# Optimization experiments

Measured on AMD Instinct MI355X. Metric: run time of the kernel, lower is better.

The kernel has to match this reference:

```python
import jax, jax.numpy as jnp
import numpy as np

N_SEND = 12288   # 12 * 32^2
N_REC = 49152    # 12 * 64^2
E = 196608       # 4 * N_REC (knn with k=4)
D = 256
EIN, EOUT = 4, 256
LIN_IN, LIN_OUT = 512, 256
B = 2


def setup_inputs() -> dict:
    key = jax.random.key(0)
    ks = jax.random.split(key, 12)
    s = 0.05
    x = jax.random.normal(ks[0], (B, N_SEND, D), jnp.float32)
    edge_attr = jax.random.normal(ks[1], (E, EIN), jnp.float32)
    idx_send = jax.random.randint(ks[2], (E,), 0, N_SEND, dtype=jnp.int32)
    idx_rec = jnp.sort(jax.random.randint(ks[3], (E,), 0, N_REC, dtype=jnp.int32))
    return {
        "x": x,
        "edge_attr": edge_attr,
        "idx_send": idx_send,
        "idx_rec": idx_rec,
        "We1": jax.random.normal(ks[4], (EIN, EOUT), jnp.float32) * s,
        "be1": jnp.zeros((EOUT,), jnp.float32),
        "We2": jax.random.normal(ks[5], (EOUT, EOUT), jnp.float32) * s,
        "be2": jnp.zeros((EOUT,), jnp.float32),
        "Wl1": jax.random.normal(ks[6], (LIN_IN, LIN_OUT), jnp.float32) * s,
        "bl1": jnp.zeros((LIN_OUT,), jnp.float32),
        "Wl2": jax.random.normal(ks[7], (LIN_OUT, LIN_OUT), jnp.float32) * s,
        "bl2": jnp.zeros((LIN_OUT,), jnp.float32),
    }


def reference(x, edge_attr, idx_send, idx_rec, We1, be1, We2, be2, Wl1, bl1, Wl2, bl2):
    # edge embedder MLP: Linear -> GELU -> Linear   [E, EOUT]
    ef = jax.nn.gelu(edge_attr @ We1 + be1) @ We2 + be2
    # gather sender node features by edge           [B, E, D]
    v_s = x[:, idx_send, :]
    # concat gathered features with (batch-broadcast) edge embeddings [B, E, D+EOUT]
    ef_b = jnp.broadcast_to(ef[None], (v_s.shape[0],) + ef.shape)
    v_s_prime = jnp.concatenate([v_s, ef_b], axis=-1)
    # scatter_sum over receiver index along edge dim -> [B, N_REC, LIN_IN]
    agg = jax.vmap(lambda m: jax.ops.segment_sum(m, idx_rec, num_segments=N_REC))(v_s_prime)
    # final FeedForward: Linear -> GELU -> Linear
    return jax.nn.gelu(agg @ Wl1 + bl1) @ Wl2 + bl2
```

## Files before the change

kernel.cpp:

```cpp
#include <hip/hip_runtime.h>
#include <hip/hip_bf16.h>

#define N_SEND 12288
#define N_REC  49152
#define NEDGE  196608
#define RECV   48

typedef __attribute__((ext_vector_type(8)))  short short8;
typedef __attribute__((ext_vector_type(4)))  short shortx4;
typedef __attribute__((ext_vector_type(4)))  float floatx4;
typedef __attribute__((ext_vector_type(16))) float floatx16;
typedef __attribute__((ext_vector_type(4)))  unsigned int uintx4;

__device__ inline short f2bs(float f) {
    __hip_bfloat16 h = __float2bfloat16(f);
    return *reinterpret_cast<short*>(&h);
}
__device__ inline float gelu_tanh(float x) {
    const float k0 = 0.7978845608028654f;
    float u = k0 * (x + 0.044715f * x * x * x);
    float e = __expf(2.0f * u);
    float t = 1.0f - 2.0f / (e + 1.0f);
    return 0.5f * x * (1.0f + t);
}

__global__ void prep_kernel(const float* __restrict__ We2, const float* __restrict__ be2,
                            const float* __restrict__ Wl1, const float* __restrict__ Wl2,
                            short* __restrict__ BT1, short* __restrict__ WT2,
                            float* __restrict__ cvec) {
    int i = blockIdx.x;
    int n = threadIdx.x;
    if (i < 256) {
        float acc = 0.f;
        for (int j = 0; j < 256; ++j)
            acc += We2[i * 256 + j] * Wl1[(256 + j) * 256 + n];
        BT1[n * 512 + i]       = f2bs(Wl1[i * 256 + n]);
        BT1[n * 512 + 256 + i] = f2bs(acc);
        WT2[n * 256 + i]       = f2bs(Wl2[i * 256 + n]);
    } else {
        float acc = 0.f;
        for (int j = 0; j < 256; ++j)
            acc += be2[j] * Wl1[(256 + j) * 256 + n];
        cvec[n] = acc;
    }
}

__global__ void xcast_kernel(const float* __restrict__ X, short* __restrict__ Xb) {
    int i = (blockIdx.x * 256 + threadIdx.x) * 8;
    floatx4 v0 = *(const floatx4*)(X + i);
    floatx4 v1 = *(const floatx4*)(X + i + 4);
    short8 p;
#pragma unroll
    for (int j = 0; j < 4; ++j) { p[j] = f2bs(v0[j]); p[j + 4] = f2bs(v1[j]); }
    *(short8*)(Xb + i) = p;
}

__global__ void bounds_kernel(const int* __restrict__ idx_rec, int* __restrict__ bnd) {
    int r = blockIdx.x * 256 + threadIdx.x;
    if (r > N_REC) return;
    int lo = 0, hi = NEDGE;
    while (lo < hi) { int mid = (lo + hi) >> 1; if (idx_rec[mid] < r) lo = mid + 1; else hi = mid; }
    bnd[r] = lo;
}

#define XTU(f, row) ((((f) * 96) + ((row) ^ ((f) & 7))) * 8)
#define HTU(f, rl)  ((((f) * 48) + ((rl) ^ ((f) & 7))) * 8)

__global__ __launch_bounds__(512, 4)
void fused48(const int* __restrict__ idx_send, const int* __restrict__ bnd,
             const float* __restrict__ EA, const float* __restrict__ We1,
             const float* __restrict__ be1, const short* __restrict__ Xb,
             const short* __restrict__ BT1, const short* __restrict__ WT2,
             const float* __restrict__ cvec, const float* __restrict__ bl1,
             const float* __restrict__ bl2, float* __restrict__ OUT) {
    __shared__ __attribute__((aligned(16))) short XT[32 * 96 * 8];
    __shared__ __attribute__((aligned(16))) short HT[32 * 48 * 8];
    __shared__ int sb[RECV + 1];

    int t = threadIdx.x;
    int r0 = blockIdx.x * RECV;
    if (t <= RECV) sb[t] = bnd[r0 + t];
    __syncthreads();

    {
        int cg = t & 31;
        int b  = (t >> 5) & 1;
        int rh = t >> 6;
        int c8 = cg * 8;
        int hc = c8 + 4 * b;

        floatx4 w0 = *(const floatx4*)(We1 + hc);
        floatx4 w1 = *(const floatx4*)(We1 + 256 + hc);
        floatx4 w2 = *(const floatx4*)(We1 + 512 + hc);
        floatx4 w3 = *(const floatx4*)(We1 + 768 + hc);
        floatx4 bb = *(const floatx4*)(be1 + hc);
        const short* xb_t = Xb + (size_t)b * N_SEND * 256 + c8;

#pragma unroll
        for (int r = 0; r < 6; ++r) {
            int rl = rh * 6 + r;
            int es = __builtin_amdgcn_readfirstlane(sb[rl]);
            int ee = __builtin_amdgcn_readfirstlane(sb[rl + 1]);

            float xacc[8];
            float hacc[4];
#pragma unroll
            for (int c = 0; c < 8; ++c) xacc[c] = 0.f;
#pragma unroll
            for (int c = 0; c < 4; ++c) hacc[c] = 0.f;

            int s = 0; floatx4 a = {0.f, 0.f, 0.f, 0.f};
            if (es < ee) { s = idx_send[es]; a = *(const floatx4*)(EA + (size_t)es * 4); }
            for (int e = es; e < ee; ++e) {
                int cs = s; floatx4 ca = a;
                int ep = (e + 1 < ee) ? e + 1 : e;
                s = idx_send[ep];
                a = *(const floatx4*)(EA + (size_t)ep * 4);
                uintx4 xv = *(const uintx4*)(xb_t + (size_t)cs * 256);
#pragma unroll
                for (int dw = 0; dw < 4; ++dw) {
                    xacc[2 * dw]     += __builtin_bit_cast(float, xv[dw] << 16);
                    xacc[2 * dw + 1] += __builtin_bit_cast(float, xv[dw] & 0xffff0000u);
                }
#pragma unroll
                for (int j = 0; j < 4; ++j) {
                    float u = ca[0] * w0[j] + ca[1] * w1[j] + ca[2] * w2[j] + ca[3] * w3[j] + bb[j];
                    hacc[j] += gelu_tanh(u);
                }
            }
            short8 xp;
#pragma unroll
            for (int c = 0; c < 8; ++c) xp[c] = f2bs(xacc[c]);
            *(short8*)(XT + XTU(cg, b * RECV + rl)) = xp;
            shortx4 hp;
#pragma unroll
            for (int c = 0; c < 4; ++c) hp[c] = f2bs(hacc[c]);
            *(shortx4*)(HT + HTU(cg, rl) + 4 * b) = hp;
        }
    }
    __syncthreads();

    int w = t >> 6, lane = t & 63;
    int m = lane & 31, q = lane >> 5;
    int wcol = w * 32;
    floatx16 acc[3];
#pragma unroll
    for (int i = 0; i < 3; ++i)
#pragma unroll
        for (int j = 0; j < 16; ++j) acc[i][j] = 0.f;

    const short* Bp1 = BT1 + (size_t)(wcol + m) * 512 + q * 8;
#pragma unroll
    for (int ci = 0; ci < 8; ++ci) {
#pragma unroll
        for (int kk = 0; kk < 4; ++kk) {
            short8 bv = *(const short8*)(Bp1 + ci * 64 + kk * 16);
            int f = ci * 8 + 2 * kk + q;
            short8 a0, a1, a2;
            if (ci < 4) {
                a0 = *(const short8*)(XT + XTU(f, m));
                a1 = *(const short8*)(XT + XTU(f, 32 + m));
                a2 = *(const short8*)(XT + XTU(f, 64 + m));
            } else {
                int fh = f - 32;
                a0 = *(const short8*)(HT + HTU(fh, m));
                int rl1 = (m < 16) ? 32 + m : m - 16;
                a1 = *(const short8*)(HT + HTU(fh, rl1));
                a2 = *(const short8*)(HT + HTU(fh, 16 + m));
            }
            acc[0] = __builtin_amdgcn_mfma_f32_32x32x16_bf16(bv, a0, acc[0], 0, 0, 0);
            acc[1] = __builtin_amdgcn_mfma_f32_32x32x16_bf16(bv, a1, acc[1], 0, 0, 0);
            acc[2] = __builtin_amdgcn_mfma_f32_32x32x16_bf16(bv, a2, acc[2], 0, 0, 0);
        }
    }
    __syncthreads();

#pragma unroll
    for (int qd = 0; qd < 4; ++qd) {
        int c0 = wcol + qd * 8 + q * 4;
        floatx4 cv  = *(const floatx4*)(cvec + c0);
        floatx4 b1v = *(const floatx4*)(bl1 + c0);
#pragma unroll
        for (int rt = 0; rt < 3; ++rt) {
            int r = rt * 32 + m;
            int bat = (r >= RECV) ? 1 : 0;
            int rl = r - RECV * bat;
            float cntv = (float)(sb[rl + 1] - sb[rl]);
            shortx4 pk;
#pragma unroll
            for (int j = 0; j < 4; ++j)
                pk[j] = f2bs(gelu_tanh(acc[rt][qd * 4 + j] + cntv * cv[j] + b1v[j]));
            *(shortx4*)(XT + XTU(w * 4 + qd, r) + q * 4) = pk;
        }
    }
#pragma unroll
    for (int i = 0; i < 3; ++i)
#pragma unroll
        for (int j = 0; j < 16; ++j) acc[i][j] = 0.f;
    __syncthreads();

    const short* Bp2 = WT2 + (size_t)(wcol + m) * 256 + q * 8;
#pragma unroll
    for (int ci = 0; ci < 4; ++ci) {
#pragma unroll
        for (int kk = 0; kk < 4; ++kk) {
            short8 bv = *(const short8*)(Bp2 + ci * 64 + kk * 16);
            int f2 = ci * 8 + 2 * kk + q;
            short8 a0 = *(const short8*)(XT + XTU(f2, m));
            short8 a1 = *(const short8*)(XT + XTU(f2, 32 + m));
            short8 a2 = *(const short8*)(XT + XTU(f2, 64 + m));
            acc[0] = __builtin_amdgcn_mfma_f32_32x32x16_bf16(bv, a0, acc[0], 0, 0, 0);
            acc[1] = __builtin_amdgcn_mfma_f32_32x32x16_bf16(bv, a1, acc[1], 0, 0, 0);
            acc[2] = __builtin_amdgcn_mfma_f32_32x32x16_bf16(bv, a2, acc[2], 0, 0, 0);
        }
    }

#pragma unroll
    for (int rt = 0; rt < 3; ++rt) {
        int r = rt * 32 + m;
        int bat = (r >= RECV) ? 1 : 0;
        int rl = r - RECV * bat;
        size_t obase = ((size_t)bat * N_REC + r0 + rl) * 256;
#pragma unroll
        for (int qd = 0; qd < 4; ++qd) {
            int c0 = wcol + qd * 8 + q * 4;
            floatx4 bv = *(const floatx4*)(bl2 + c0);
            floatx4 o;
#pragma unroll
            for (int j = 0; j < 4; ++j)
                o[j] = acc[rt][qd * 4 + j] + bv[j];
            *(floatx4*)(OUT + obase + c0) = o;
        }
    }
}

extern "C" void kernel_launch(void* const* d_in, const int* in_sizes, int n_in,
                              void* d_out, int out_size, void* d_ws, size_t ws_size,
                              hipStream_t stream) {
    const float* x        = (const float*)d_in[0];
    const float* ea       = (const float*)d_in[1];
    const int*   idx_send = (const int*)d_in[2];
    const int*   idx_rec  = (const int*)d_in[3];
    const float* We1      = (const float*)d_in[4];
    const float* be1      = (const float*)d_in[5];
    const float* We2      = (const float*)d_in[6];
    const float* be2      = (const float*)d_in[7];
    const float* Wl1      = (const float*)d_in[8];
    const float* bl1      = (const float*)d_in[9];
    const float* Wl2      = (const float*)d_in[10];
    const float* bl2      = (const float*)d_in[11];
    float* out = (float*)d_out;
    char*  ws  = (char*)d_ws;

    short* BT1  = (short*)(ws + 0);
    short* WT2  = (short*)(ws + 262144);
    float* cvec = (float*)(ws + 393216);
    int*   bnd  = (int*)  (ws + 397312);
    short* Xb   = (short*)(ws + 1048576);

    prep_kernel<<<257, 256, 0, stream>>>(We2, be2, Wl1, Wl2, BT1, WT2, cvec);
    xcast_kernel<<<(2 * N_SEND * 256) / (256 * 8), 256, 0, stream>>>(x, Xb);
    bounds_kernel<<<(N_REC + 1 + 255) / 256, 256, 0, stream>>>(idx_rec, bnd);
    fused48<<<N_REC / RECV, 512, 0, stream>>>(idx_send, bnd, ea, We1, be1, Xb,
                                              BT1, WT2, cvec, bl1, bl2, out);
}
```

Before: 280.5 us.

## Flatten per-receiver edge loops into double-buffered 4-edge batches with interleaved X layout

Replaces the per-receiver edge loop, which prefetched one edge ahead, with a single flattened loop over all edges of a thread's six receivers. Edges are loaded in double-buffered batches of four, and partial sums are flushed to shared memory at receiver boundaries. The bf16 copy of x is also re-laid out so both batches of a sender node sit next to each other in one 512-element row, which improves gather locality. The aim is more memory-level parallelism for the irregular gathers, at the cost of more registers, boundary branching, and possible occupancy loss.

```diff
diff --git a/kernel.cpp b/kernel.cpp
--- a/kernel.cpp
+++ b/kernel.cpp
@@ -47,12 +47,16 @@
 
 __global__ void xcast_kernel(const float* __restrict__ X, short* __restrict__ Xb) {
     int i = (blockIdx.x * 256 + threadIdx.x) * 8;
+    int row = i >> 8;
+    int c   = i & 255;
+    int bb_ = (row >= N_SEND) ? 1 : 0;
+    int n   = row - bb_ * N_SEND;
     floatx4 v0 = *(const floatx4*)(X + i);
     floatx4 v1 = *(const floatx4*)(X + i + 4);
     short8 p;
 #pragma unroll
     for (int j = 0; j < 4; ++j) { p[j] = f2bs(v0[j]); p[j + 4] = f2bs(v1[j]); }
-    *(short8*)(Xb + i) = p;
+    *(short8*)(Xb + (size_t)n * 512 + bb_ * 256 + c) = p;
 }
 
 __global__ void bounds_kernel(const int* __restrict__ idx_rec, int* __restrict__ bnd) {
@@ -75,7 +79,7 @@
              const float* __restrict__ bl2, float* __restrict__ OUT) {
     __shared__ __attribute__((aligned(16))) short XT[32 * 96 * 8];
     __shared__ __attribute__((aligned(16))) short HT[32 * 48 * 8];
-    __shared__ int sb[RECV + 1];
+    __shared__ int sb[RECV + 9];
 
     int t = threadIdx.x;
     int r0 = blockIdx.x * RECV;
@@ -94,49 +98,91 @@
         floatx4 w2 = *(const floatx4*)(We1 + 512 + hc);
         floatx4 w3 = *(const floatx4*)(We1 + 768 + hc);
         floatx4 bb = *(const floatx4*)(be1 + hc);
-        const short* xb_t = Xb + (size_t)b * N_SEND * 256 + c8;
-
-#pragma unroll
-        for (int r = 0; r < 6; ++r) {
-            int rl = rh * 6 + r;
-            int es = __builtin_amdgcn_readfirstlane(sb[rl]);
-            int ee = __builtin_amdgcn_readfirstlane(sb[rl + 1]);
-
-            float xacc[8];
-            float hacc[4];
-#pragma unroll
-            for (int c = 0; c < 8; ++c) xacc[c] = 0.f;
-#pragma unroll
-            for (int c = 0; c < 4; ++c) hacc[c] = 0.f;
-
-            int s = 0; floatx4 a = {0.f, 0.f, 0.f, 0.f};
-            if (es < ee) { s = idx_send[es]; a = *(const floatx4*)(EA + (size_t)es * 4); }
-            for (int e = es; e < ee; ++e) {
-                int cs = s; floatx4 ca = a;
-                int ep = (e + 1 < ee) ? e + 1 : e;
-                s = idx_send[ep];
-                a = *(const floatx4*)(EA + (size_t)ep * 4);
-                uintx4 xv = *(const uintx4*)(xb_t + (size_t)cs * 256);
-#pragma unroll
-                for (int dw = 0; dw < 4; ++dw) {
-                    xacc[2 * dw]     += __builtin_bit_cast(float, xv[dw] << 16);
-                    xacc[2 * dw + 1] += __builtin_bit_cast(float, xv[dw] & 0xffff0000u);
-                }
-#pragma unroll
-                for (int j = 0; j < 4; ++j) {
-                    float u = ca[0] * w0[j] + ca[1] * w1[j] + ca[2] * w2[j] + ca[3] * w3[j] + bb[j];
-                    hacc[j] += gelu_tanh(u);
-                }
+        const short* xb_t = Xb + b * 256 + c8;
+
+        int rl0 = rh * 6;
+        int e0 = __builtin_amdgcn_readfirstlane(sb[rl0]);
+        int eN = __builtin_amdgcn_readfirstlane(sb[rl0 + 6]);
+
+        float xacc[8];
+        float hacc[4];
+#pragma unroll
+        for (int c = 0; c < 8; ++c) xacc[c] = 0.f;
+#pragma unroll
+        for (int c = 0; c < 4; ++c) hacc[c] = 0.f;
+
+        int rcur = rl0;
+        int bend = __builtin_amdgcn_readfirstlane(sb[rcur + 1]);
+
+#define FLUSH_R() {                                                          \
+        short8 xp_; shortx4 hp_;                                             \
+        _Pragma("unroll")                                                    \
+        for (int c_ = 0; c_ < 8; ++c_) xp_[c_] = f2bs(xacc[c_]);             \
+        *(short8*)(XT + XTU(cg, b * RECV + rcur)) = xp_;                     \
+        _Pragma("unroll")                                                    \
+        for (int c_ = 0; c_ < 4; ++c_) hp_[c_] = f2bs(hacc[c_]);             \
+        *(shortx4*)(HT + HTU(cg, rcur) + 4 * b) = hp_;                       \
+        _Pragma("unroll")                                                    \
+        for (int c_ = 0; c_ < 8; ++c_) xacc[c_] = 0.f;                       \
+        _Pragma("unroll")                                                    \
+        for (int c_ = 0; c_ < 4; ++c_) hacc[c_] = 0.f;                       \
+        ++rcur;                                                              \
+        bend = __builtin_amdgcn_readfirstlane(sb[rcur + 1]);                 \
+    }
+
+#define LOADC(S, A, XV, base) {                                              \
+        _Pragma("unroll")                                                    \
+        for (int j_ = 0; j_ < 4; ++j_) {                                     \
+            int ei_ = (base) + j_; ei_ = (ei_ < eN) ? ei_ : (eN - 1);        \
+            S[j_] = idx_send[ei_];                                           \
+            A[j_] = *(const floatx4*)(EA + (size_t)ei_ * 4);                 \
+        }                                                                    \
+        _Pragma("unroll")                                                    \
+        for (int j_ = 0; j_ < 4; ++j_)                                       \
+            XV[j_] = *(const uintx4*)(xb_t + (size_t)S[j_] * 512);           \
+    }
+
+#define CONSUME1(av, xvv, ej) {                                              \
+        if ((ej) < eN) {                                                     \
+            while ((ej) == bend) FLUSH_R();                                  \
+            uintx4 xv_ = (xvv);                                              \
+            _Pragma("unroll")                                                \
+            for (int dw_ = 0; dw_ < 4; ++dw_) {                              \
+                xacc[2 * dw_]     += __builtin_bit_cast(float, xv_[dw_] << 16);          \
+                xacc[2 * dw_ + 1] += __builtin_bit_cast(float, xv_[dw_] & 0xffff0000u);  \
+            }                                                                \
+            floatx4 a_ = (av);                                               \
+            _Pragma("unroll")                                                \
+            for (int jj_ = 0; jj_ < 4; ++jj_) {                              \
+                float u_ = a_[0] * w0[jj_] + a_[1] * w1[jj_] + a_[2] * w2[jj_] \
+                         + a_[3] * w3[jj_] + bb[jj_];                        \
+                hacc[jj_] += gelu_tanh(u_);                                  \
+            }                                                                \
+        }                                                                    \
+    }
+
+        if (e0 < eN) {
+            int sA[4], sB[4];
+            floatx4 aA[4], aB[4];
+            uintx4 xvA[4], xvB[4];
+            int e = e0;
+            LOADC(sA, aA, xvA, e);
+            for (;;) {
+                int moreB = (e + 4 < eN);
+                if (moreB) LOADC(sB, aB, xvB, e + 4);
+#pragma unroll
+                for (int j = 0; j < 4; ++j) CONSUME1(aA[j], xvA[j], e + j);
+                e += 4;
+                if (!moreB) break;
+                int moreA = (e + 4 < eN);
+                if (moreA) LOADC(sA, aA, xvA, e + 4);
+#pragma unroll
+                for (int j = 0; j < 4; ++j) CONSUME1(aB[j], xvB[j], e + j);
+                e += 4;
+                if (!moreA) break;
             }
-            short8 xp;
-#pragma unroll
-            for (int c = 0; c < 8; ++c) xp[c] = f2bs(xacc[c]);
-            *(short8*)(XT + XTU(cg, b * RECV + rl)) = xp;
-            shortx4 hp;
-#pragma unroll
-            for (int c = 0; c < 4; ++c) hp[c] = f2bs(hacc[c]);
-            *(shortx4*)(HT + HTU(cg, rl) + 4 * b) = hp;
-        }
+        }
+        while (rcur < rl0 + 6) FLUSH_R();
     }
     __syncthreads();
 
```

New measurement: 274.6 us. 2.1% less time.

## Shrink receiver tile to 16 and interleave batch rows in bf16 node buffer

Applied to the files above, without the earlier changes.

The fused kernel now handles 16 receivers per block instead of 48, so each wave keeps a single 32x32 MFMA tile (16 receivers times 2 batches) and uses a third of the LDS and accumulator registers. The occupancy hint rises to 8 blocks per CU and the grid grows threefold. The bf16 cast of x is also rearranged so both batch rows of a sender node sit next to each other, which places the two gathers for an edge in one 1KB span. In exchange, the GEMM weight matrices are reloaded from global or L2 three times as often per output row, and there are more block launches and barrier overheads.

```diff
diff --git a/kernel.cpp b/kernel.cpp
--- a/kernel.cpp
+++ b/kernel.cpp
@@ -4,7 +4,7 @@
 #define N_SEND 12288
 #define N_REC  49152
 #define NEDGE  196608
-#define RECV   48
+#define RECV   16
 
 typedef __attribute__((ext_vector_type(8)))  short short8;
 typedef __attribute__((ext_vector_type(4)))  short shortx4;
@@ -47,12 +47,16 @@
 
 __global__ void xcast_kernel(const float* __restrict__ X, short* __restrict__ Xb) {
     int i = (blockIdx.x * 256 + threadIdx.x) * 8;
+    int row = i >> 8;
+    int c   = i & 255;
+    int bb_ = (row >= N_SEND) ? 1 : 0;
+    int n   = row - bb_ * N_SEND;
     floatx4 v0 = *(const floatx4*)(X + i);
     floatx4 v1 = *(const floatx4*)(X + i + 4);
     short8 p;
 #pragma unroll
     for (int j = 0; j < 4; ++j) { p[j] = f2bs(v0[j]); p[j + 4] = f2bs(v1[j]); }
-    *(short8*)(Xb + i) = p;
+    *(short8*)(Xb + (size_t)n * 512 + bb_ * 256 + c) = p;
 }
 
 __global__ void bounds_kernel(const int* __restrict__ idx_rec, int* __restrict__ bnd) {
@@ -63,18 +67,18 @@
     bnd[r] = lo;
 }
 
-#define XTU(f, row) ((((f) * 96) + ((row) ^ ((f) & 7))) * 8)
-#define HTU(f, rl)  ((((f) * 48) + ((rl) ^ ((f) & 7))) * 8)
-
-__global__ __launch_bounds__(512, 4)
-void fused48(const int* __restrict__ idx_send, const int* __restrict__ bnd,
+#define XTU(f, row) ((((f) * 32) + ((row) ^ ((f) & 7))) * 8)
+#define HTU(f, rl)  ((((f) * 16) + ((rl) ^ ((f) & 7))) * 8)
+
+__global__ __launch_bounds__(512, 8)
+void fused16(const int* __restrict__ idx_send, const int* __restrict__ bnd,
              const float* __restrict__ EA, const float* __restrict__ We1,
              const float* __restrict__ be1, const short* __restrict__ Xb,
              const short* __restrict__ BT1, const short* __restrict__ WT2,
              const float* __restrict__ cvec, const float* __restrict__ bl1,
              const float* __restrict__ bl2, float* __restrict__ OUT) {
-    __shared__ __attribute__((aligned(16))) short XT[32 * 96 * 8];
-    __shared__ __attribute__((aligned(16))) short HT[32 * 48 * 8];
+    __shared__ __attribute__((aligned(16))) short XT[32 * 32 * 8];
+    __shared__ __attribute__((aligned(16))) short HT[32 * 16 * 8];
     __shared__ int sb[RECV + 1];
 
     int t = threadIdx.x;
@@ -94,11 +98,11 @@
         floatx4 w2 = *(const floatx4*)(We1 + 512 + hc);
         floatx4 w3 = *(const floatx4*)(We1 + 768 + hc);
         floatx4 bb = *(const floatx4*)(be1 + hc);
-        const short* xb_t = Xb + (size_t)b * N_SEND * 256 + c8;
-
-#pragma unroll
-        for (int r = 0; r < 6; ++r) {
-            int rl = rh * 6 + r;
+        const short* xb_t = Xb + b * 256 + c8;
+
+#pragma unroll
+        for (int r = 0; r < 2; ++r) {
+            int rl = rh * 2 + r;
             int es = __builtin_amdgcn_readfirstlane(sb[rl]);
             int ee = __builtin_amdgcn_readfirstlane(sb[rl + 1]);
 
@@ -116,7 +120,7 @@
                 int ep = (e + 1 < ee) ? e + 1 : e;
                 s = idx_send[ep];
                 a = *(const floatx4*)(EA + (size_t)ep * 4);
-                uintx4 xv = *(const uintx4*)(xb_t + (size_t)cs * 256);
+                uintx4 xv = *(const uintx4*)(xb_t + (size_t)cs * 512);
 #pragma unroll
                 for (int dw = 0; dw < 4; ++dw) {
                     xacc[2 * dw]     += __builtin_bit_cast(float, xv[dw] << 16);
@@ -143,11 +147,9 @@
     int w = t >> 6, lane = t & 63;
     int m = lane & 31, q = lane >> 5;
     int wcol = w * 32;
-    floatx16 acc[3];
-#pragma unroll
-    for (int i = 0; i < 3; ++i)
-#pragma unroll
-        for (int j = 0; j < 16; ++j) acc[i][j] = 0.f;
+    floatx16 acc;
+#pragma unroll
+    for (int j = 0; j < 16; ++j) acc[j] = 0.f;
 
     const short* Bp1 = BT1 + (size_t)(wcol + m) * 512 + q * 8;
 #pragma unroll
@@ -156,47 +158,34 @@
         for (int kk = 0; kk < 4; ++kk) {
             short8 bv = *(const short8*)(Bp1 + ci * 64 + kk * 16);
             int f = ci * 8 + 2 * kk + q;
-            short8 a0, a1, a2;
+            short8 a0;
             if (ci < 4) {
                 a0 = *(const short8*)(XT + XTU(f, m));
-                a1 = *(const short8*)(XT + XTU(f, 32 + m));
-                a2 = *(const short8*)(XT + XTU(f, 64 + m));
             } else {
-                int fh = f - 32;
-                a0 = *(const short8*)(HT + HTU(fh, m));
-                int rl1 = (m < 16) ? 32 + m : m - 16;
-                a1 = *(const short8*)(HT + HTU(fh, rl1));
-                a2 = *(const short8*)(HT + HTU(fh, 16 + m));
+                a0 = *(const short8*)(HT + HTU(f - 32, m & 15));
             }
-            acc[0] = __builtin_amdgcn_mfma_f32_32x32x16_bf16(bv, a0, acc[0], 0, 0, 0);
-            acc[1] = __builtin_amdgcn_mfma_f32_32x32x16_bf16(bv, a1, acc[1], 0, 0, 0);
-            acc[2] = __builtin_amdgcn_mfma_f32_32x32x16_bf16(bv, a2, acc[2], 0, 0, 0);
-        }
-    }
-    __syncthreads();
-
-#pragma unroll
-    for (int qd = 0; qd < 4; ++qd) {
-        int c0 = wcol + qd * 8 + q * 4;
-        floatx4 cv  = *(const floatx4*)(cvec + c0);
-        floatx4 b1v = *(const floatx4*)(bl1 + c0);
-#pragma unroll
-        for (int rt = 0; rt < 3; ++rt) {
-            int r = rt * 32 + m;
-            int bat = (r >= RECV) ? 1 : 0;
-            int rl = r - RECV * bat;
-            float cntv = (float)(sb[rl + 1] - sb[rl]);
+            acc = __builtin_amdgcn_mfma_f32_32x32x16_bf16(bv, a0, acc, 0, 0, 0);
+        }
+    }
+    __syncthreads();
+
+    {
+        int rl = m & 15;
+        float cntv = (float)(sb[rl + 1] - sb[rl]);
+#pragma unroll
+        for (int qd = 0; qd < 4; ++qd) {
+            int c0 = wcol + qd * 8 + q * 4;
+            floatx4 cv  = *(const floatx4*)(cvec + c0);
+            floatx4 b1v = *(const floatx4*)(bl1 + c0);
             shortx4 pk;
 #pragma unroll
             for (int j = 0; j < 4; ++j)
-                pk[j] = f2bs(gelu_tanh(acc[rt][qd * 4 + j] + cntv * cv[j] + b1v[j]));
-            *(shortx4*)(XT + XTU(w * 4 + qd, r) + q * 4) = pk;
-        }
-    }
-#pragma unroll
-    for (int i = 0; i < 3; ++i)
-#pragma unroll
-        for (int j = 0; j < 16; ++j) acc[i][j] = 0.f;
+                pk[j] = f2bs(gelu_tanh(acc[qd * 4 + j] + cntv * cv[j] + b1v[j]));
+            *(shortx4*)(XT + XTU(w * 4 + qd, m) + q * 4) = pk;
+        }
+#pragma unroll
+        for (int j = 0; j < 16; ++j) acc[j] = 0.f;
+    }
     __syncthreads();
 
     const short* Bp2 = WT2 + (size_t)(wcol + m) * 256 + q * 8;
@@ -207,19 +196,13 @@
             short8 bv = *(const short8*)(Bp2 + ci * 64 + kk * 16);
             int f2 = ci * 8 + 2 * kk + q;
             short8 a0 = *(const short8*)(XT + XTU(f2, m));
-            short8 a1 = *(const short8*)(XT + XTU(f2, 32 + m));
-            short8 a2 = *(const short8*)(XT + XTU(f2, 64 + m));
-            acc[0] = __builtin_amdgcn_mfma_f32_32x32x16_bf16(bv, a0, acc[0], 0, 0, 0);
-            acc[1] = __builtin_amdgcn_mfma_f32_32x32x16_bf16(bv, a1, acc[1], 0, 0, 0);
-            acc[2] = __builtin_amdgcn_mfma_f32_32x32x16_bf16(bv, a2, acc[2], 0, 0, 0);
-        }
-    }
-
-#pragma unroll
-    for (int rt = 0; rt < 3; ++rt) {
-        int r = rt * 32 + m;
-        int bat = (r >= RECV) ? 1 : 0;
-        int rl = r - RECV * bat;
+            acc = __builtin_amdgcn_mfma_f32_32x32x16_bf16(bv, a0, acc, 0, 0, 0);
+        }
+    }
+
+    {
+        int bat = m >> 4;
+        int rl = m & 15;
         size_t obase = ((size_t)bat * N_REC + r0 + rl) * 256;
 #pragma unroll
         for (int qd = 0; qd < 4; ++qd) {
@@ -228,7 +211,7 @@
             floatx4 o;
 #pragma unroll
             for (int j = 0; j < 4; ++j)
-                o[j] = acc[rt][qd * 4 + j] + bv[j];
+                o[j] = acc[qd * 4 + j] + bv[j];
             *(floatx4*)(OUT + obase + c0) = o;
         }
     }
@@ -261,6 +244,6 @@
     prep_kernel<<<257, 256, 0, stream>>>(We2, be2, Wl1, Wl2, BT1, WT2, cvec);
     xcast_kernel<<<(2 * N_SEND * 256) / (256 * 8), 256, 0, stream>>>(x, Xb);
     bounds_kernel<<<(N_REC + 1 + 255) / 256, 256, 0, stream>>>(idx_rec, bnd);
-    fused48<<<N_REC / RECV, 512, 0, stream>>>(idx_send, bnd, ea, We1, be1, Xb,
+    fused16<<<N_REC / RECV, 512, 0, stream>>>(idx_send, bnd, ea, We1, be1, Xb,
                                               BT1, WT2, cvec, bl1, bl2, out);
 }
```

After: 331.9 us. 1.18x slower.

## Interleave batches in bf16 X layout and stage output through LDS

Applied to the files above, without the earlier changes.

The bf16 copy of x is now stored as [N_SEND][batch][256], so the two batch gathers for one sender land in adjacent memory and share cache lines. The epilogue no longer writes MFMA accumulators straight to global memory with strided 16-byte stores. It stages each batch's 48x256 fp32 tile in a swizzled LDS buffer that reuses XT, then writes fully coalesced rows. This costs extra barriers and LDS traffic, and relies on XT being large enough to hold 48*256 floats.

```diff
diff --git a/kernel.cpp b/kernel.cpp
--- a/kernel.cpp
+++ b/kernel.cpp
@@ -47,12 +47,16 @@
 
 __global__ void xcast_kernel(const float* __restrict__ X, short* __restrict__ Xb) {
     int i = (blockIdx.x * 256 + threadIdx.x) * 8;
+    int row = i >> 8;
+    int c   = i & 255;
+    int bb_ = (row >= N_SEND) ? 1 : 0;
+    int n   = row - bb_ * N_SEND;
     floatx4 v0 = *(const floatx4*)(X + i);
     floatx4 v1 = *(const floatx4*)(X + i + 4);
     short8 p;
 #pragma unroll
     for (int j = 0; j < 4; ++j) { p[j] = f2bs(v0[j]); p[j + 4] = f2bs(v1[j]); }
-    *(short8*)(Xb + i) = p;
+    *(short8*)(Xb + (size_t)n * 512 + bb_ * 256 + c) = p;
 }
 
 __global__ void bounds_kernel(const int* __restrict__ idx_rec, int* __restrict__ bnd) {
@@ -94,7 +98,7 @@
         floatx4 w2 = *(const floatx4*)(We1 + 512 + hc);
         floatx4 w3 = *(const floatx4*)(We1 + 768 + hc);
         floatx4 bb = *(const floatx4*)(be1 + hc);
-        const short* xb_t = Xb + (size_t)b * N_SEND * 256 + c8;
+        const short* xb_t = Xb + b * 256 + c8;
 
 #pragma unroll
         for (int r = 0; r < 6; ++r) {
@@ -116,7 +120,7 @@
                 int ep = (e + 1 < ee) ? e + 1 : e;
                 s = idx_send[ep];
                 a = *(const floatx4*)(EA + (size_t)ep * 4);
-                uintx4 xv = *(const uintx4*)(xb_t + (size_t)cs * 256);
+                uintx4 xv = *(const uintx4*)(xb_t + (size_t)cs * 512);
 #pragma unroll
                 for (int dw = 0; dw < 4; ++dw) {
                     xacc[2 * dw]     += __builtin_bit_cast(float, xv[dw] << 16);
@@ -214,22 +218,41 @@
             acc[2] = __builtin_amdgcn_mfma_f32_32x32x16_bf16(bv, a2, acc[2], 0, 0, 0);
         }
     }
-
-#pragma unroll
-    for (int rt = 0; rt < 3; ++rt) {
-        int r = rt * 32 + m;
-        int bat = (r >= RECV) ? 1 : 0;
-        int rl = r - RECV * bat;
-        size_t obase = ((size_t)bat * N_REC + r0 + rl) * 256;
-#pragma unroll
-        for (int qd = 0; qd < 4; ++qd) {
-            int c0 = wcol + qd * 8 + q * 4;
-            floatx4 bv = *(const floatx4*)(bl2 + c0);
-            floatx4 o;
-#pragma unroll
-            for (int j = 0; j < 4; ++j)
-                o[j] = acc[rt][qd * 4 + j] + bv[j];
-            *(floatx4*)(OUT + obase + c0) = o;
+    __syncthreads();
+
+    {
+        float* XF = (float*)XT;
+#pragma unroll
+        for (int p = 0; p < 2; ++p) {
+#pragma unroll
+            for (int rt = 0; rt < 3; ++rt) {
+                int r = rt * 32 + m;
+                if (r >= 48 * p && r < 48 * p + 48) {
+                    int row = r - 48 * p;
+                    int sw = (row & 7) * 4;
+#pragma unroll
+                    for (int qd = 0; qd < 4; ++qd) {
+                        int c0 = wcol + qd * 8 + q * 4;
+                        floatx4 bv = *(const floatx4*)(bl2 + c0);
+                        floatx4 o;
+#pragma unroll
+                        for (int j = 0; j < 4; ++j)
+                            o[j] = acc[rt][qd * 4 + j] + bv[j];
+                        *(floatx4*)(XF + row * 256 + (c0 ^ sw)) = o;
+                    }
+                }
+            }
+            __syncthreads();
+#pragma unroll
+            for (int k = 0; k < 6; ++k) {
+                int cid = t + k * 512;
+                int row = cid >> 6;
+                int cc  = (cid & 63) * 4;
+                int sw  = (row & 7) * 4;
+                floatx4 v = *(const floatx4*)(XF + row * 256 + (cc ^ sw));
+                *(floatx4*)(OUT + ((size_t)p * N_REC + r0 + row) * 256 + cc) = v;
+            }
+            if (p == 0) __syncthreads();
         }
     }
 }
```

Result: faster. 271.7 us (-3.2%).
